# Optimization experiments

Measured on AMD Instinct MI355X. Metric: run time of the kernel, lower is better.

Reference implementation:

```python
import jax, jax.numpy as jnp
import numpy as np

N_NODE = 200000   # item catalog size (n_node)
EMB = 100         # emb_size
NNZ = 1000000     # hypergraph adjacency nonzeros
B = 1024          # batch / cl_size
L = 50            # session length
LAYERS = 2        # HyperConv layers (opt.layer)
TAU = 0.2         # contrastive temperature
K_NEI = 3         # FindNeighbors.neighbor_n


def setup_inputs() -> dict:
    key = jax.random.key(0)
    ks = jax.random.split(key, 16)
    g = 1.414 / np.sqrt(EMB)  # xavier_normal gain=1.414 scale
    inp = {}
    inp["embedding"] = jax.random.normal(ks[0], (N_NODE, EMB), jnp.float32) * 0.1
    inp["adj_val"] = jax.random.uniform(ks[1], (NNZ,), jnp.float32)
    inp["A"] = jax.random.uniform(ks[2], (B, B), jnp.float32) * 0.01
    inp["D"] = jax.random.uniform(ks[3], (B, B), jnp.float32) * 0.01
    inp["z2"] = jax.random.normal(ks[4], (B, EMB), jnp.float32)
    inp["Wcf1"] = jax.random.normal(ks[5], (EMB, EMB), jnp.float32) * g
    inp["bcf1"] = jnp.zeros((EMB,), jnp.float32)
    inp["Wcf2"] = jax.random.normal(ks[6], (EMB, EMB), jnp.float32) * g
    inp["bcf2"] = jnp.zeros((EMB,), jnp.float32)
    inp["Wkg1"] = jax.random.normal(ks[7], (EMB, EMB), jnp.float32) * g
    inp["bkg1"] = jnp.zeros((EMB,), jnp.float32)
    inp["Wkg2"] = jax.random.normal(ks[8], (EMB, EMB), jnp.float32) * g
    inp["bkg2"] = jnp.zeros((EMB,), jnp.float32)
    inp["session_len"] = jnp.full((B, 1), float(L), jnp.float32)
    inp["adj_row"] = jax.random.randint(ks[9], (NNZ,), 0, N_NODE, jnp.int32)
    inp["adj_col"] = jax.random.randint(ks[10], (NNZ,), 0, N_NODE, jnp.int32)
    inp["items"] = jax.random.randint(ks[11], (B, L), 0, N_NODE + 1, jnp.int32)
    return inp


def _proj(z, W1, b1, W2, b2):
    # nn.Linear -> ELU -> nn.Linear (Contrast_2view projector)
    return jax.nn.elu(z @ W1.T + b1) @ W2.T + b2


def reference(embedding, adj_val, A, D, z2,
              Wcf1, bcf1, Wcf2, bcf2, Wkg1, bkg1, Wkg2, bkg2,
              session_len, adj_row, adj_col, items):
    # ---- HyperConv: layered sparse propagation, averaged over layers ----
    h = embedding
    acc = embedding
    for _ in range(LAYERS):
        # torch.sparse.mm(adjacency, h) via gather + segment_sum
        h = jax.ops.segment_sum(adj_val[:, None] * h[adj_col], adj_row,
                                num_segments=N_NODE)
        acc = acc + h
    hyper = acc / (LAYERS + 1)  # [N_NODE, EMB]

    # ---- RelationGAT.forward ----
    emb_pad = jnp.concatenate([jnp.zeros((1, EMB), hyper.dtype), hyper], axis=0)
    seq_h = emb_pad[items]                       # [B, L, EMB]
    rel = jnp.sum(seq_h, axis=1) / session_len   # [B, EMB]
    rel = (D @ A) @ rel                          # session-graph conv
    c = jax.nn.selu(rel)
    l_c = c / jnp.linalg.norm(c, axis=-1, keepdims=True)  # [B, EMB]

    # ---- FindNeighbors (dropout omitted: eval mode) ----
    sess = l_c
    norms = jnp.sqrt(jnp.sum(sess * sess + 1e-6, axis=1, keepdims=True))
    cos = (sess @ sess.T) / (norms @ norms.T)    # [B, B]
    cos = jax.nn.softmax(cos, axis=-1)
    topv, topi = jax.lax.top_k(cos, K_NEI)       # [B, K]
    topv = jax.nn.softmax(topv, axis=-1)
    neighbor = jnp.sum(topv[:, :, None] * sess[topi], axis=1)  # [B, EMB]

    # ---- Contrast_2view ----
    z1p = _proj(sess, Wcf1, bcf1, Wcf2, bcf2)
    z2p = _proj(z2, Wkg1, bkg1, Wkg2, bkg2)
    n1 = jnp.linalg.norm(z1p, axis=-1, keepdims=True)
    n2 = jnp.linalg.norm(z2p, axis=-1, keepdims=True)
    simm = jnp.exp((z1p @ z2p.T) / (n1 @ n2.T) / TAU)
    simm = simm / (jnp.sum(simm, axis=1, keepdims=True) + 1e-8)
    cl_loss = -jnp.mean(jnp.log(jnp.diagonal(simm)))  # pos = eye

    return hyper, l_c, neighbor, cl_loss
```

## Files before the change

### kernel.cpp

```cpp
#include <hip/hip_runtime.h>
#include <hip/hip_bf16.h>

#define N_NODE 200000
#define EMB 100
#define NNZ 1000000
#define BATCH 1024
#define SLEN 50
#define BE (BATCH * EMB)
#define SCAN_BLK 1024
#define PROJ_ROWS 8
#define UNR 8

#define OFF_LC    20000000LL
#define OFF_NB    20102400LL
#define OFF_LOSS  20204800LL

typedef __hip_bfloat16 bf16;

__device__ __forceinline__ float b2f(bf16 x) { return __bfloat162float(x); }
__device__ __forceinline__ bf16 f2b(float x) { return __float2bfloat16(x); }

__device__ __forceinline__ float ldf(const void* p, long long i, int f32) {
    return f32 ? ((const float*)p)[i] : b2f(((const bf16*)p)[i]);
}
__device__ __forceinline__ void stf(void* p, long long i, int f32, float v) {
    if (f32) ((float*)p)[i] = v;
    else     ((bf16*)p)[i] = f2b(v);
}

__device__ __forceinline__ float bfb2f(unsigned short s) {
    return __uint_as_float(((unsigned)s) << 16);
}
__device__ __forceinline__ unsigned short f2bfb(float x) {
    bf16 h = f2b(x); unsigned short r; __builtin_memcpy(&r, &h, 2); return r;
}
__device__ __forceinline__ float2 up2(unsigned u) {
    return make_float2(bfb2f((unsigned short)(u & 0xffff)), bfb2f((unsigned short)(u >> 16)));
}
__device__ __forceinline__ unsigned pk2(float a, float b) {
    return (unsigned)f2bfb(a) | ((unsigned)f2bfb(b) << 16);
}
__device__ __forceinline__ float2 ldf2(const void* p, long long pi, int f32) {
    if (f32) return ((const float2*)p)[pi];
    return up2(((const unsigned*)p)[pi]);
}
template<bool F32>
__device__ __forceinline__ float2 ldf2t(const void* p, long long pi) {
    if (F32) return ((const float2*)p)[pi];
    return up2(((const unsigned*)p)[pi]);
}
__device__ __forceinline__ void stf2(void* p, long long pi, int f32, float a, float b) {
    if (f32) ((float2*)p)[pi] = make_float2(a, b);
    else     ((unsigned*)p)[pi] = pk2(a, b);
}

__device__ __forceinline__ float wave_allreduce_sum(float v) {
    for (int m = 32; m > 0; m >>= 1) v += __shfl_xor(v, m, 64);
    return v;
}

__global__ void hist_kernel(const int* __restrict__ rows, int* __restrict__ counts,
                            const void* __restrict__ adjval, int* __restrict__ flag) {
    if (blockIdx.x == 0 && threadIdx.x == 0) {
        int f = 0;
        const bf16* p = (const bf16*)adjval;
        for (int i = 0; i < 64; i++) {
            float x = b2f(p[i]);
            if (!(x >= 0.0f && x <= 1.0f)) f = 1;
        }
        *flag = f;
    }
    int e = blockIdx.x * 256 + threadIdx.x;
    if (e < NNZ) atomicAdd(&counts[rows[e]], 1);
}

__global__ void scan_block(const int* __restrict__ counts, int* __restrict__ incl,
                           int* __restrict__ bsums) {
    __shared__ int s[SCAN_BLK];
    int i = blockIdx.x * SCAN_BLK + threadIdx.x;
    int v = (i < N_NODE) ? counts[i] : 0;
    s[threadIdx.x] = v;
    __syncthreads();
    for (int off = 1; off < SCAN_BLK; off <<= 1) {
        int add = (threadIdx.x >= (unsigned)off) ? s[threadIdx.x - off] : 0;
        __syncthreads();
        s[threadIdx.x] += add;
        __syncthreads();
    }
    if (i < N_NODE) incl[i] = s[threadIdx.x];
    if (threadIdx.x == SCAN_BLK - 1) bsums[blockIdx.x] = s[threadIdx.x];
}

__global__ void scan_top(int* __restrict__ bsums, int nb) {
    __shared__ int s[256];
    int t = threadIdx.x;
    int v = (t < nb) ? bsums[t] : 0;
    s[t] = v;
    __syncthreads();
    for (int off = 1; off < 256; off <<= 1) {
        int add = (t >= off) ? s[t - off] : 0;
        __syncthreads();
        s[t] += add;
        __syncthreads();
    }
    if (t < nb) bsums[t] = s[t] - v;
}

__global__ void scan_add(const int* __restrict__ counts, const int* __restrict__ incl,
                         const int* __restrict__ bsums, int* __restrict__ row_ptr,
                         int* __restrict__ cursor) {
    int i = blockIdx.x * SCAN_BLK + threadIdx.x;
    if (i < N_NODE) {
        int ex = incl[i] - counts[i] + bsums[blockIdx.x];
        row_ptr[i] = ex;
        cursor[i] = ex;
    }
    if (i == 0) row_ptr[N_NODE] = NNZ;
}

__global__ void permute_edges(const int* __restrict__ arow, const int* __restrict__ acol,
                              const void* __restrict__ aval, int* __restrict__ cursor,
                              int2* __restrict__ cv, const int* __restrict__ flagp) {
    const int f32 = *flagp;
    int e = blockIdx.x * 256 + threadIdx.x;
    if (e >= NNZ) return;
    int r = arow[e];
    int pos = atomicAdd(&cursor[r], 1);
    float v = ldf(aval, e, f32);
    cv[pos] = make_int2(acol[e], __float_as_int(v));
}

template<bool F32>
__device__ __forceinline__ void spmm1_body(
        const int* __restrict__ rp, const int2* __restrict__ cv,
        const void* __restrict__ emb, unsigned* __restrict__ h1) {
    int lane = threadIdx.x & 63;
    int r = blockIdx.x * 4 + (threadIdx.x >> 6);
    if (r >= N_NODE || lane >= 50) return;
    int k0 = rp[r], k1 = rp[r + 1];
    float a0 = 0.f, a1 = 0.f;
    for (int k = k0; k < k1; k += UNR) {
        int2 c[UNR];
        #pragma unroll
        for (int j = 0; j < UNR; j++) {
            int kk = k + j;
            c[j] = cv[kk < k1 ? kk : k1 - 1];
        }
        float2 e[UNR];
        #pragma unroll
        for (int j = 0; j < UNR; j++)
            e[j] = ldf2t<F32>(emb, (long long)c[j].x * 50 + lane);
        #pragma unroll
        for (int j = 0; j < UNR; j++) {
            float v = (k + j < k1) ? __int_as_float(c[j].y) : 0.f;
            a0 += v * e[j].x; a1 += v * e[j].y;
        }
    }
    h1[(long long)r * 50 + lane] = pk2(a0, a1);
}

__global__ __launch_bounds__(256) void spmm_gather1(
        const int* __restrict__ rp, const int2* __restrict__ cv,
        const void* __restrict__ emb,
        unsigned* __restrict__ h1, const int* __restrict__ flagp) {
    if (*flagp) spmm1_body<true>(rp, cv, emb, h1);
    else        spmm1_body<false>(rp, cv, emb, h1);
}

template<bool F32>
__device__ __forceinline__ void spmm2_body(
        const int* __restrict__ rp, const int2* __restrict__ cv,
        const void* __restrict__ emb,
        const unsigned* __restrict__ h1, void* __restrict__ out) {
    int lane = threadIdx.x & 63;
    int r = blockIdx.x * 4 + (threadIdx.x >> 6);
    if (r >= N_NODE || lane >= 50) return;
    int k0 = rp[r], k1 = rp[r + 1];
    float a0 = 0.f, a1 = 0.f;
    for (int k = k0; k < k1; k += UNR) {
        int2 c[UNR];
        #pragma unroll
        for (int j = 0; j < UNR; j++) {
            int kk = k + j;
            c[j] = cv[kk < k1 ? kk : k1 - 1];
        }
        float2 e[UNR];
        #pragma unroll
        for (int j = 0; j < UNR; j++)
            e[j] = up2(h1[(long long)c[j].x * 50 + lane]);
        #pragma unroll
        for (int j = 0; j < UNR; j++) {
            float v = (k + j < k1) ? __int_as_float(c[j].y) : 0.f;
            a0 += v * e[j].x; a1 += v * e[j].y;
        }
    }
    float2 eb = ldf2t<F32>(emb, (long long)r * 50 + lane);
    float2 h1r = up2(h1[(long long)r * 50 + lane]);
    stf2(out, (long long)r * 50 + lane, F32 ? 1 : 0,
         (eb.x + h1r.x + a0) * (1.0f / 3.0f), (eb.y + h1r.y + a1) * (1.0f / 3.0f));
}

__global__ __launch_bounds__(256) void spmm_gather2(
        const int* __restrict__ rp, const int2* __restrict__ cv,
        const void* __restrict__ emb,
        const unsigned* __restrict__ h1, void* __restrict__ out,
        const int* __restrict__ flagp) {
    if (*flagp) spmm2_body<true>(rp, cv, emb, h1, out);
    else        spmm2_body<false>(rp, cv, emb, h1, out);
}

template<bool F32>
__device__ __forceinline__ void rel_rows_body(
        const void* __restrict__ out, const int* __restrict__ items,
        const void* __restrict__ slen, float* __restrict__ rel) {
    int lane = threadIdx.x & 63;
    int b = blockIdx.x * 4 + (threadIdx.x >> 6);
    if (b >= BATCH || lane >= 50) return;
    float s0 = 0.f, s1 = 0.f;
    #pragma unroll
    for (int l0 = 0; l0 < SLEN; l0 += 10) {
        int it[10];
        #pragma unroll
        for (int j = 0; j < 10; j++) it[j] = items[b * SLEN + l0 + j];
        float2 e[10];
        #pragma unroll
        for (int j = 0; j < 10; j++) {
            int idx = (it[j] > 0) ? it[j] - 1 : 0;
            e[j] = ldf2t<F32>(out, (long long)idx * 50 + lane);
        }
        #pragma unroll
        for (int j = 0; j < 10; j++) {
            float m = (it[j] > 0) ? 1.f : 0.f;
            s0 += m * e[j].x; s1 += m * e[j].y;
        }
    }
    float inv = 1.0f / ldf(slen, b, F32 ? 1 : 0);
    ((float2*)rel)[b * 50 + lane] = make_float2(s0 * inv, s1 * inv);
}

__global__ __launch_bounds__(256) void rel_rows(
        const void* __restrict__ out, const int* __restrict__ items,
        const void* __restrict__ slen, float* __restrict__ rel,
        const int* __restrict__ flagp) {
    if (*flagp) rel_rows_body<true>(out, items, slen, rel);
    else        rel_rows_body<false>(out, items, slen, rel);
}

__global__ __launch_bounds__(256) void bmm_rows(const void* __restrict__ M,
                                                const float* __restrict__ X,
                                                float* __restrict__ Y,
                                                const int* __restrict__ flagp) {
    __shared__ float ms[4][BATCH];
    const int f32 = *flagp;
    int i0 = blockIdx.x * 4;
    int t = threadIdx.x;
    for (int idx = t; idx < 4 * BATCH; idx += 256) {
        int rr = idx >> 10, j = idx & 1023;
        ms[rr][j] = ldf(M, (long long)(i0 + rr) * BATCH + j, f32);
    }
    __syncthreads();
    int w = t >> 6, lane = t & 63;
    if (lane >= 50) return;
    int i = i0 + w;
    const float2* X2 = (const float2*)X;
    float s0 = 0.f, s1 = 0.f;
    for (int j = 0; j < BATCH; j++) {
        float m = ms[w][j];
        float2 x = X2[j * 50 + lane];
        s0 += m * x.x; s1 += m * x.y;
    }
    ((float2*)Y)[i * 50 + lane] = make_float2(s0, s1);
}

__global__ void selu_norm(const float* __restrict__ rel2, float* __restrict__ sess,
                          float* __restrict__ sessT, float* __restrict__ ns,
                          void* __restrict__ out, const int* __restrict__ flagp) {
    const int f32 = *flagp;
    int b = blockIdx.x, t = threadIdx.x;
    const float sc = 1.0507009873554804934193349852946f;
    const float al = 1.6732632423543772848170429916717f;
    float x0 = (t < EMB) ? rel2[b * EMB + t] : 0.f;
    float x1 = (t + 64 < EMB) ? rel2[b * EMB + t + 64] : 0.f;
    float c0 = (x0 > 0.f) ? sc * x0 : sc * (al * expm1f(x0));
    float c1 = (x1 > 0.f) ? sc * x1 : sc * (al * expm1f(x1));
    if (t >= EMB) c0 = 0.f;
    if (t + 64 >= EMB) c1 = 0.f;
    float nrm = sqrtf(wave_allreduce_sum(c0 * c0 + c1 * c1));
    float l0 = c0 / nrm, l1 = c1 / nrm;
    float nterm = 0.f;
    if (t < EMB) {
        sess[b * EMB + t] = l0;
        sessT[t * BATCH + b] = l0;
        stf(out, OFF_LC + b * EMB + t, f32, l0);
        nterm += l0 * l0 + 1e-6f;
    }
    if (t + 64 < EMB) {
        sess[b * EMB + t + 64] = l1;
        sessT[(t + 64) * BATCH + b] = l1;
        stf(out, OFF_LC + b * EMB + t + 64, f32, l1);
        nterm += l1 * l1 + 1e-6f;
    }
    float n2sum = wave_allreduce_sum(nterm);
    if (t == 0) ns[b] = sqrtf(n2sum);
}

__global__ void neighbor_kernel(const float* __restrict__ sess, const float* __restrict__ sessT,
                                const float* __restrict__ ns, void* __restrict__ out,
                                const int* __restrict__ flagp) {
    __shared__ float si[EMB];
    __shared__ float red[4];
    __shared__ float wrv[4]; __shared__ int wri[4];
    __shared__ float chv[3]; __shared__ int chi[3];
    __shared__ float stv[3];
    const int f32 = *flagp;
    int i = blockIdx.x, t = threadIdx.x;
    if (t < EMB) si[t] = sess[i * EMB + t];
    __syncthreads();
    float ni = ns[i];
    float d0 = 0.f, d1 = 0.f, d2 = 0.f, d3 = 0.f;
    for (int k = 0; k < EMB; k++) {
        float sv = si[k];
        const float* row = sessT + k * BATCH;
        d0 += sv * row[t];
        d1 += sv * row[t + 256];
        d2 += sv * row[t + 512];
        d3 += sv * row[t + 768];
    }
    float pv0 = expf(d0 / (ni * ns[t]));
    float pv1 = expf(d1 / (ni * ns[t + 256]));
    float pv2 = expf(d2 / (ni * ns[t + 512]));
    float pv3 = expf(d3 / (ni * ns[t + 768]));
    float local = pv0 + pv1 + pv2 + pv3;
    float w = wave_allreduce_sum(local);
    if ((t & 63) == 0) red[t >> 6] = w;
    __syncthreads();
    float S = red[0] + red[1] + red[2] + red[3];

    int c0 = -1, c1 = -1, c2 = -1;
    float pv[4] = {pv0, pv1, pv2, pv3};
    for (int r = 0; r < 3; r++) {
        float bv = -1e30f; int bi = 0x7fffffff;
        #pragma unroll
        for (int m = 0; m < 4; m++) {
            int j = t + (m << 8);
            if (j == c0 || j == c1 || j == c2) continue;
            float v = pv[m];
            if (v > bv || (v == bv && j < bi)) { bv = v; bi = j; }
        }
        #pragma unroll
        for (int off = 1; off < 64; off <<= 1) {
            float ov = __shfl_xor(bv, off);
            int oi = __shfl_xor(bi, off);
            if (ov > bv || (ov == bv && oi < bi)) { bv = ov; bi = oi; }
        }
        if ((t & 63) == 0) { wrv[t >> 6] = bv; wri[t >> 6] = bi; }
        __syncthreads();
        if (t == 0) {
            float fv = wrv[0]; int fi = wri[0];
            for (int wq = 1; wq < 4; wq++) {
                if (wrv[wq] > fv || (wrv[wq] == fv && wri[wq] < fi)) { fv = wrv[wq]; fi = wri[wq]; }
            }
            chv[r] = fv; chi[r] = fi;
        }
        __syncthreads();
        if (r == 0) c0 = chi[0];
        else if (r == 1) c1 = chi[1];
        else c2 = chi[2];
    }
    if (t == 0) {
        float e0 = expf(chv[0] / S), e1 = expf(chv[1] / S), e2 = expf(chv[2] / S);
        float es = e0 + e1 + e2;
        stv[0] = e0 / es; stv[1] = e1 / es; stv[2] = e2 / es;
    }
    __syncthreads();
    if (t < EMB) {
        float o = stv[0] * sess[chi[0] * EMB + t]
                + stv[1] * sess[chi[1] * EMB + t]
                + stv[2] * sess[chi[2] * EMB + t];
        stf(out, OFF_NB + i * EMB + t, f32, o);
    }
}

__global__ __launch_bounds__(256) void proj2(
        const void* __restrict__ X, int x_dual,
        const void* __restrict__ W1, const void* __restrict__ B1,
        const void* __restrict__ W2, const void* __restrict__ B2,
        float* __restrict__ Z, float* __restrict__ ZT, float* __restrict__ nrm,
        const int* __restrict__ flagp) {
    __shared__ float wT[EMB * EMB];
    __shared__ float bsh[EMB];
    __shared__ float hid[PROJ_ROWS][EMB];
    __shared__ float xr[2][EMB];
    __shared__ float red2[2][2];
    const int f32 = *flagp;
    int t = threadIdx.x;
    int sub = t >> 7, u = t & 127;
    int r0 = blockIdx.x * PROJ_ROWS;
    for (int idx = t; idx < EMB * EMB; idx += 256) {
        int o = idx / EMB, k = idx - o * EMB;
        wT[k * EMB + o] = ldf(W1, idx, f32);
    }
    if (t < EMB) bsh[t] = ldf(B1, t, f32);
    __syncthreads();
    for (int pr = 0; pr < PROJ_ROWS; pr += 2) {
        int row = r0 + pr + sub;
        if (u < EMB)
            xr[sub][u] = x_dual ? ldf(X, (long long)row * EMB + u, f32)
                                : ((const float*)X)[row * EMB + u];
        __syncthreads();
        if (u < EMB) {
            float s = bsh[u];
            for (int k = 0; k < EMB; k++) s += xr[sub][k] * wT[k * EMB + u];
            hid[pr + sub][u] = (s > 0.f) ? s : expm1f(s);
        }
        __syncthreads();
    }
    for (int idx = t; idx < EMB * EMB; idx += 256) {
        int o = idx / EMB, k = idx - o * EMB;
        wT[k * EMB + o] = ldf(W2, idx, f32);
    }
    if (t < EMB) bsh[t] = ldf(B2, t, f32);
    __syncthreads();
    for (int pr = 0; pr < PROJ_ROWS; pr += 2) {
        int row = r0 + pr + sub;
        float sq = 0.f;
        if (u < EMB) {
            float o = bsh[u];
            const float* h = hid[pr + sub];
            for (int k = 0; k < EMB; k++) o += h[k] * wT[k * EMB + u];
            Z[(long long)row * EMB + u] = o;
            if (ZT) ZT[(long long)u * BATCH + row] = o;
            sq = o * o;
        }
        sq = wave_allreduce_sum(sq);
        int w = t >> 6;
        if ((t & 63) == 0) red2[sub][w & 1] = sq;
        __syncthreads();
        if (u == 0) nrm[row] = sqrtf(red2[sub][0] + red2[sub][1]);
        __syncthreads();
    }
}

__global__ void loss_kernel(const float* __restrict__ z1p, const float* __restrict__ z2pT,
                            const float* __restrict__ n1, const float* __restrict__ n2,
                            float* __restrict__ acc) {
    __shared__ float zi[EMB];
    __shared__ float red[4];
    __shared__ float sdiag;
    int i = blockIdx.x, t = threadIdx.x;
    if (t < EMB) zi[t] = z1p[i * EMB + t];
    __syncthreads();
    float ni = n1[i];
    float d0 = 0.f, d1 = 0.f, d2 = 0.f, d3 = 0.f;
    for (int k = 0; k < EMB; k++) {
        float zv = zi[k];
        const float* row = z2pT + k * BATCH;
        d0 += zv * row[t];
        d1 += zv * row[t + 256];
        d2 += zv * row[t + 512];
        d3 += zv * row[t + 768];
    }
    float e0 = expf(d0 / (ni * n2[t]) * 5.0f);
    float e1 = expf(d1 / (ni * n2[t + 256]) * 5.0f);
    float e2 = expf(d2 / (ni * n2[t + 512]) * 5.0f);
    float e3 = expf(d3 / (ni * n2[t + 768]) * 5.0f);
    if (t == (i & 255)) {
        int m = i >> 8;
        sdiag = (m == 0) ? e0 : (m == 1) ? e1 : (m == 2) ? e2 : e3;
    }
    float local = e0 + e1 + e2 + e3;
    float w = wave_allreduce_sum(local);
    if ((t & 63) == 0) red[t >> 6] = w;
    __syncthreads();
    if (t == 0) {
        float S = red[0] + red[1] + red[2] + red[3];
        float l = -logf(sdiag / (S + 1e-8f));
        atomicAdd(acc, l * (1.0f / BATCH));
    }
}

__global__ void write_loss(const float* __restrict__ acc, void* __restrict__ out,
                           const int* __restrict__ flagp) {
    stf(out, OFF_LOSS, *flagp, acc[0]);
}

extern "C" void kernel_launch(void* const* d_in, const int* in_sizes, int n_in,
                              void* d_out, int out_size, void* d_ws, size_t ws_size,
                              hipStream_t stream) {
    const void* emb  = d_in[0];
    const void* aval = d_in[1];
    const void* Amat = d_in[2];
    const void* Dmat = d_in[3];
    const void* z2   = d_in[4];
    const void* Wcf1 = d_in[5];
    const void* bcf1 = d_in[6];
    const void* Wcf2 = d_in[7];
    const void* bcf2 = d_in[8];
    const void* Wkg1 = d_in[9];
    const void* bkg1 = d_in[10];
    const void* Wkg2 = d_in[11];
    const void* bkg2 = d_in[12];
    const void* slen = d_in[13];
    const int* arow  = (const int*)d_in[14];
    const int* acol  = (const int*)d_in[15];
    const int* items = (const int*)d_in[16];

    int* flag      = (int*)d_ws;
    int* counts    = (int*)((char*)d_ws + 256);
    int* cursor    = counts;
    int* row_ptr   = counts + N_NODE;
    int* bsums     = row_ptr + N_NODE + 64;
    int2* cv       = (int2*)(bsums + 256);
    int* scanbuf   = (int*)cv;
    unsigned* h1buf = (unsigned*)(cv + NNZ);
    float* fsmall  = (float*)(h1buf + (long long)N_NODE * 50);
    float* rel   = fsmall;
    float* t1    = rel  + BE;
    float* rel2  = t1   + BE;
    float* sess  = rel2 + BE;
    float* sessT = sess + BE;
    float* z1p   = sessT + BE;
    float* z2p   = z1p  + BE;
    float* z2pT  = z2p  + BE;
    float* ns    = z2pT + BE;
    float* n1    = ns + BATCH;
    float* n2    = n1 + BATCH;
    float* lacc  = n2 + BATCH;

    const int nscan = (N_NODE + SCAN_BLK - 1) / SCAN_BLK;

    hipMemsetAsync(counts, 0, (size_t)N_NODE * sizeof(int), stream);
    hist_kernel<<<(NNZ + 255) / 256, 256, 0, stream>>>(arow, counts, aval, flag);
    scan_block<<<nscan, SCAN_BLK, 0, stream>>>(counts, scanbuf, bsums);
    scan_top<<<1, 256, 0, stream>>>(bsums, nscan);
    scan_add<<<nscan, SCAN_BLK, 0, stream>>>(counts, scanbuf, bsums, row_ptr, cursor);
    permute_edges<<<(NNZ + 255) / 256, 256, 0, stream>>>(arow, acol, aval, cursor,
                                                         cv, flag);

    spmm_gather1<<<(N_NODE + 3) / 4, 256, 0, stream>>>(row_ptr, cv, emb, h1buf, flag);
    spmm_gather2<<<(N_NODE + 3) / 4, 256, 0, stream>>>(row_ptr, cv, emb, h1buf,
                                                       d_out, flag);

    rel_rows<<<(BATCH + 3) / 4, 256, 0, stream>>>(d_out, items, slen, rel, flag);
    bmm_rows<<<BATCH / 4, 256, 0, stream>>>(Amat, rel, t1, flag);
    bmm_rows<<<BATCH / 4, 256, 0, stream>>>(Dmat, t1, rel2, flag);
    selu_norm<<<BATCH, 64, 0, stream>>>(rel2, sess, sessT, ns, d_out, flag);

    neighbor_kernel<<<BATCH, 256, 0, stream>>>(sess, sessT, ns, d_out, flag);

    proj2<<<BATCH / PROJ_ROWS, 256, 0, stream>>>(sess, 0, Wcf1, bcf1, Wcf2, bcf2,
                                                 z1p, nullptr, n1, flag);
    proj2<<<BATCH / PROJ_ROWS, 256, 0, stream>>>(z2, 1, Wkg1, bkg1, Wkg2, bkg2,
                                                 z2p, z2pT, n2, flag);
    hipMemsetAsync(lacc, 0, sizeof(float), stream);
    loss_kernel<<<BATCH, 256, 0, stream>>>(z1p, z2pT, n1, n2, lacc);
    write_loss<<<1, 1, 0, stream>>>(lacc, d_out, flag);
}
```

Measured before the change: 713.1 us.

## Make SpMM kernels persistent with software-prefetched edge batches; fuse SELU-norm into bmm

```diff
diff --git a/kernel.cpp b/kernel.cpp
--- a/kernel.cpp
+++ b/kernel.cpp
@@ -10,6 +10,7 @@
 #define SCAN_BLK 1024
 #define PROJ_ROWS 8
 #define UNR 8
+#define SPMM_BLOCKS 2048
 
 #define OFF_LC    20000000LL
 #define OFF_NB    20102400LL
@@ -130,33 +131,73 @@
     cv[pos] = make_int2(acol[e], __float_as_int(v));
 }
 
+__device__ __forceinline__ void ld_batch_cv(int2* c, const int2* __restrict__ cv,
+                                            int k0, int k1) {
+    int ke = (k1 > k0) ? (k1 - 1) : 0;
+    #pragma unroll
+    for (int j = 0; j < UNR; j++) {
+        int kk = k0 + j;
+        c[j] = cv[kk < k1 ? kk : ke];
+    }
+}
+
 template<bool F32>
 __device__ __forceinline__ void spmm1_body(
         const int* __restrict__ rp, const int2* __restrict__ cv,
         const void* __restrict__ emb, unsigned* __restrict__ h1) {
+    int nw = gridDim.x * 4;
+    int wid = blockIdx.x * 4 + (threadIdx.x >> 6);
     int lane = threadIdx.x & 63;
-    int r = blockIdx.x * 4 + (threadIdx.x >> 6);
-    if (r >= N_NODE || lane >= 50) return;
+    bool act = lane < 50;
+    int pl = act ? lane : 0;
+
+    int r = wid;
+    if (r >= N_NODE) return;
     int k0 = rp[r], k1 = rp[r + 1];
-    float a0 = 0.f, a1 = 0.f;
-    for (int k = k0; k < k1; k += UNR) {
-        int2 c[UNR];
+    int2 cc[UNR];
+    ld_batch_cv(cc, cv, k0, k1);
+    int rn = r + nw;
+    int k0n = 0, k1n = 0;
+    if (rn < N_NODE) { k0n = rp[rn]; k1n = rp[rn + 1]; }
+
+    for (;;) {
+        float2 e[UNR];
+        #pragma unroll
+        for (int j = 0; j < UNR; j++)
+            e[j] = ldf2t<F32>(emb, (long long)cc[j].x * 50 + pl);
+        int2 cn[UNR];
+        if (rn < N_NODE) ld_batch_cv(cn, cv, k0n, k1n);
+        int rnn = rn + nw;
+        int k0nn = 0, k1nn = 0;
+        if (rnn < N_NODE) { k0nn = rp[rnn]; k1nn = rp[rnn + 1]; }
+
+        float a0 = 0.f, a1 = 0.f;
         #pragma unroll
         for (int j = 0; j < UNR; j++) {
-            int kk = k + j;
-            c[j] = cv[kk < k1 ? kk : k1 - 1];
-        }
-        float2 e[UNR];
-        #pragma unroll
-        for (int j = 0; j < UNR; j++)
-            e[j] = ldf2t<F32>(emb, (long long)c[j].x * 50 + lane);
-        #pragma unroll
-        for (int j = 0; j < UNR; j++) {
-            float v = (k + j < k1) ? __int_as_float(c[j].y) : 0.f;
+            float v = (k0 + j < k1) ? __int_as_float(cc[j].y) : 0.f;
             a0 += v * e[j].x; a1 += v * e[j].y;
         }
-    }
-    h1[(long long)r * 50 + lane] = pk2(a0, a1);
+        for (int k = k0 + UNR; k < k1; k += UNR) {
+            int2 ct[UNR];
+            #pragma unroll
+            for (int j = 0; j < UNR; j++) { int kk = k + j; ct[j] = cv[kk < k1 ? kk : k1 - 1]; }
+            float2 et[UNR];
+            #pragma unroll
+            for (int j = 0; j < UNR; j++)
+                et[j] = ldf2t<F32>(emb, (long long)ct[j].x * 50 + pl);
+            #pragma unroll
+            for (int j = 0; j < UNR; j++) {
+                float v = (k + j < k1) ? __int_as_float(ct[j].y) : 0.f;
+                a0 += v * et[j].x; a1 += v * et[j].y;
+            }
+        }
+        if (act) h1[(long long)r * 50 + lane] = pk2(a0, a1);
+        if (rn >= N_NODE) return;
+        r = rn; k0 = k0n; k1 = k1n;
+        #pragma unroll
+        for (int j = 0; j < UNR; j++) cc[j] = cn[j];
+        rn = rnn; k0n = k0nn; k1n = k1nn;
+    }
 }
 
 __global__ __launch_bounds__(256) void spmm_gather1(
@@ -172,32 +213,63 @@
         const int* __restrict__ rp, const int2* __restrict__ cv,
         const void* __restrict__ emb,
         const unsigned* __restrict__ h1, void* __restrict__ out) {
+    int nw = gridDim.x * 4;
+    int wid = blockIdx.x * 4 + (threadIdx.x >> 6);
     int lane = threadIdx.x & 63;
-    int r = blockIdx.x * 4 + (threadIdx.x >> 6);
-    if (r >= N_NODE || lane >= 50) return;
+    bool act = lane < 50;
+    int pl = act ? lane : 0;
+
+    int r = wid;
+    if (r >= N_NODE) return;
     int k0 = rp[r], k1 = rp[r + 1];
-    float a0 = 0.f, a1 = 0.f;
-    for (int k = k0; k < k1; k += UNR) {
-        int2 c[UNR];
+    int2 cc[UNR];
+    ld_batch_cv(cc, cv, k0, k1);
+    int rn = r + nw;
+    int k0n = 0, k1n = 0;
+    if (rn < N_NODE) { k0n = rp[rn]; k1n = rp[rn + 1]; }
+
+    for (;;) {
+        float2 ebv = ldf2t<F32>(emb, (long long)r * 50 + pl);
+        float2 h1r = up2(h1[(long long)r * 50 + pl]);
+        float2 e[UNR];
+        #pragma unroll
+        for (int j = 0; j < UNR; j++)
+            e[j] = up2(h1[(long long)cc[j].x * 50 + pl]);
+        int2 cn[UNR];
+        if (rn < N_NODE) ld_batch_cv(cn, cv, k0n, k1n);
+        int rnn = rn + nw;
+        int k0nn = 0, k1nn = 0;
+        if (rnn < N_NODE) { k0nn = rp[rnn]; k1nn = rp[rnn + 1]; }
+
+        float a0 = 0.f, a1 = 0.f;
         #pragma unroll
         for (int j = 0; j < UNR; j++) {
-            int kk = k + j;
-            c[j] = cv[kk < k1 ? kk : k1 - 1];
-        }
-        float2 e[UNR];
-        #pragma unroll
-        for (int j = 0; j < UNR; j++)
-            e[j] = up2(h1[(long long)c[j].x * 50 + lane]);
-        #pragma unroll
-        for (int j = 0; j < UNR; j++) {
-            float v = (k + j < k1) ? __int_as_float(c[j].y) : 0.f;
+            float v = (k0 + j < k1) ? __int_as_float(cc[j].y) : 0.f;
             a0 += v * e[j].x; a1 += v * e[j].y;
         }
-    }
-    float2 eb = ldf2t<F32>(emb, (long long)r * 50 + lane);
-    float2 h1r = up2(h1[(long long)r * 50 + lane]);
-    stf2(out, (long long)r * 50 + lane, F32 ? 1 : 0,
-         (eb.x + h1r.x + a0) * (1.0f / 3.0f), (eb.y + h1r.y + a1) * (1.0f / 3.0f));
+        for (int k = k0 + UNR; k < k1; k += UNR) {
+            int2 ct[UNR];
+            #pragma unroll
+            for (int j = 0; j < UNR; j++) { int kk = k + j; ct[j] = cv[kk < k1 ? kk : k1 - 1]; }
+            float2 et[UNR];
+            #pragma unroll
+            for (int j = 0; j < UNR; j++)
+                et[j] = up2(h1[(long long)ct[j].x * 50 + pl]);
+            #pragma unroll
+            for (int j = 0; j < UNR; j++) {
+                float v = (k + j < k1) ? __int_as_float(ct[j].y) : 0.f;
+                a0 += v * et[j].x; a1 += v * et[j].y;
+            }
+        }
+        if (act)
+            stf2(out, (long long)r * 50 + lane, F32 ? 1 : 0,
+                 (ebv.x + h1r.x + a0) * (1.0f / 3.0f), (ebv.y + h1r.y + a1) * (1.0f / 3.0f));
+        if (rn >= N_NODE) return;
+        r = rn; k0 = k0n; k1 = k1n;
+        #pragma unroll
+        for (int j = 0; j < UNR; j++) cc[j] = cn[j];
+        rn = rnn; k0n = k0nn; k1n = k1nn;
+    }
 }
 
 __global__ __launch_bounds__(256) void spmm_gather2(
@@ -246,10 +318,15 @@
     else        rel_rows_body<false>(out, items, slen, rel);
 }
 
-__global__ __launch_bounds__(256) void bmm_rows(const void* __restrict__ M,
-                                                const float* __restrict__ X,
-                                                float* __restrict__ Y,
-                                                const int* __restrict__ flagp) {
+template<int MODE>
+__global__ __launch_bounds__(256) void bmm_rows_t(const void* __restrict__ M,
+                                                  const float* __restrict__ X,
+                                                  float* __restrict__ Y,
+                                                  float* __restrict__ sess,
+                                                  float* __restrict__ sessT,
+                                                  float* __restrict__ ns,
+                                                  void* __restrict__ out,
+                                                  const int* __restrict__ flagp) {
     __shared__ float ms[4][BATCH];
     const int f32 = *flagp;
     int i0 = blockIdx.x * 4;
@@ -260,48 +337,37 @@
     }
     __syncthreads();
     int w = t >> 6, lane = t & 63;
-    if (lane >= 50) return;
+    bool act = lane < 50;
     int i = i0 + w;
-    const float2* X2 = (const float2*)X;
     float s0 = 0.f, s1 = 0.f;
-    for (int j = 0; j < BATCH; j++) {
-        float m = ms[w][j];
-        float2 x = X2[j * 50 + lane];
-        s0 += m * x.x; s1 += m * x.y;
-    }
-    ((float2*)Y)[i * 50 + lane] = make_float2(s0, s1);
-}
-
-__global__ void selu_norm(const float* __restrict__ rel2, float* __restrict__ sess,
-                          float* __restrict__ sessT, float* __restrict__ ns,
-                          void* __restrict__ out, const int* __restrict__ flagp) {
-    const int f32 = *flagp;
-    int b = blockIdx.x, t = threadIdx.x;
+    if (act) {
+        const float2* X2 = (const float2*)X;
+        for (int j = 0; j < BATCH; j++) {
+            float m = ms[w][j];
+            float2 x = X2[j * 50 + lane];
+            s0 += m * x.x; s1 += m * x.y;
+        }
+    }
+    if (MODE == 0) {
+        if (act) ((float2*)Y)[i * 50 + lane] = make_float2(s0, s1);
+        return;
+    }
     const float sc = 1.0507009873554804934193349852946f;
     const float al = 1.6732632423543772848170429916717f;
-    float x0 = (t < EMB) ? rel2[b * EMB + t] : 0.f;
-    float x1 = (t + 64 < EMB) ? rel2[b * EMB + t + 64] : 0.f;
-    float c0 = (x0 > 0.f) ? sc * x0 : sc * (al * expm1f(x0));
-    float c1 = (x1 > 0.f) ? sc * x1 : sc * (al * expm1f(x1));
-    if (t >= EMB) c0 = 0.f;
-    if (t + 64 >= EMB) c1 = 0.f;
+    float c0 = (s0 > 0.f) ? sc * s0 : sc * (al * expm1f(s0));
+    float c1 = (s1 > 0.f) ? sc * s1 : sc * (al * expm1f(s1));
+    if (!act) { c0 = 0.f; c1 = 0.f; }
     float nrm = sqrtf(wave_allreduce_sum(c0 * c0 + c1 * c1));
     float l0 = c0 / nrm, l1 = c1 / nrm;
-    float nterm = 0.f;
-    if (t < EMB) {
-        sess[b * EMB + t] = l0;
-        sessT[t * BATCH + b] = l0;
-        stf(out, OFF_LC + b * EMB + t, f32, l0);
-        nterm += l0 * l0 + 1e-6f;
-    }
-    if (t + 64 < EMB) {
-        sess[b * EMB + t + 64] = l1;
-        sessT[(t + 64) * BATCH + b] = l1;
-        stf(out, OFF_LC + b * EMB + t + 64, f32, l1);
-        nterm += l1 * l1 + 1e-6f;
-    }
+    float nterm = act ? (l0 * l0 + l1 * l1 + 2e-6f) : 0.f;
     float n2sum = wave_allreduce_sum(nterm);
-    if (t == 0) ns[b] = sqrtf(n2sum);
+    if (act) {
+        ((float2*)sess)[i * 50 + lane] = make_float2(l0, l1);
+        sessT[(2 * lane) * BATCH + i] = l0;
+        sessT[(2 * lane + 1) * BATCH + i] = l1;
+        stf2(out, OFF_LC / 2 + (long long)i * 50 + lane, f32, l0, l1);
+    }
+    if (lane == 0) ns[i] = sqrtf(n2sum);
 }
 
 __global__ void neighbor_kernel(const float* __restrict__ sess, const float* __restrict__ sessT,
@@ -516,8 +582,7 @@
     float* fsmall  = (float*)(h1buf + (long long)N_NODE * 50);
     float* rel   = fsmall;
     float* t1    = rel  + BE;
-    float* rel2  = t1   + BE;
-    float* sess  = rel2 + BE;
+    float* sess  = t1   + BE;
     float* sessT = sess + BE;
     float* z1p   = sessT + BE;
     float* z2p   = z1p  + BE;
@@ -537,14 +602,15 @@
     permute_edges<<<(NNZ + 255) / 256, 256, 0, stream>>>(arow, acol, aval, cursor,
                                                          cv, flag);
 
-    spmm_gather1<<<(N_NODE + 3) / 4, 256, 0, stream>>>(row_ptr, cv, emb, h1buf, flag);
-    spmm_gather2<<<(N_NODE + 3) / 4, 256, 0, stream>>>(row_ptr, cv, emb, h1buf,
-                                                       d_out, flag);
+    spmm_gather1<<<SPMM_BLOCKS, 256, 0, stream>>>(row_ptr, cv, emb, h1buf, flag);
+    spmm_gather2<<<SPMM_BLOCKS, 256, 0, stream>>>(row_ptr, cv, emb, h1buf,
+                                                  d_out, flag);
 
     rel_rows<<<(BATCH + 3) / 4, 256, 0, stream>>>(d_out, items, slen, rel, flag);
-    bmm_rows<<<BATCH / 4, 256, 0, stream>>>(Amat, rel, t1, flag);
-    bmm_rows<<<BATCH / 4, 256, 0, stream>>>(Dmat, t1, rel2, flag);
-    selu_norm<<<BATCH, 64, 0, stream>>>(rel2, sess, sessT, ns, d_out, flag);
+    bmm_rows_t<0><<<BATCH / 4, 256, 0, stream>>>(Amat, rel, t1,
+                                                 nullptr, nullptr, nullptr, nullptr, flag);
+    bmm_rows_t<1><<<BATCH / 4, 256, 0, stream>>>(Dmat, t1, nullptr,
+                                                 sess, sessT, ns, d_out, flag);
 
     neighbor_kernel<<<BATCH, 256, 0, stream>>>(sess, sessT, ns, d_out, flag);
 
```

Result: slower. 740.7 us (+3.9%).
